# Kernel tuning notes

Hardware: AMD Instinct MI355X
Metric: run time of the kernel (lower is better)

The kernel has to match this reference:

```python
import jax, jax.numpy as jnp
import numpy as np

TEMPERATURE = 0.5

def setup_inputs() -> dict:
    key = jax.random.key(0)
    ks = jax.random.split(key, 8)
    B, D, H, T, C = 4096, 1024, 4096, 8, 1000
    return {
        "x": jax.random.normal(ks[0], (B, D), jnp.float32),
        "signatures": jax.random.normal(ks[1], (T, D), jnp.float32) * 0.1,
        "W_up": jax.random.normal(ks[2], (T, H, D), jnp.float32) * (1.0 / np.sqrt(D)),
        "b_up": jax.random.normal(ks[3], (T, H), jnp.float32) * 0.01,
        "W_down": jax.random.normal(ks[4], (T, D, H), jnp.float32) * (1.0 / np.sqrt(H)),
        "b_down": jax.random.normal(ks[5], (T, D), jnp.float32) * 0.01,
        "W_cls": jax.random.normal(ks[6], (C, D), jnp.float32) * (1.0 / np.sqrt(D)),
        "b_cls": jax.random.normal(ks[7], (C,), jnp.float32) * 0.01,
    }

def reference(x, signatures, W_up, b_up, W_down, b_down, W_cls, b_cls):
    # Soft routing: scores (B, T), softmax weights at temperature 0.5
    scores = x @ signatures.T
    indices = jnp.argmax(scores, axis=-1)
    weights = jax.nn.softmax(scores / TEMPERATURE, axis=-1)
    # Batched per-tile FFN: Linear -> GELU(exact) -> Linear, all tiles at once
    h = jax.nn.gelu(jnp.einsum('bd,thd->bth', x, W_up) + b_up[None], approximate=False)  # (B,T,H)
    tile_out = jnp.einsum('bth,tdh->btd', h, W_down) + b_down[None]                      # (B,T,D)
    # Weighted combine + residual
    outputs = jnp.einsum('bt,btd->bd', weights, tile_out) + x
    logits = outputs @ W_cls.T + b_cls
    return logits, indices, weights
```

## Files before the change

### kernel.cpp

```cpp
#include <hip/hip_runtime.h>
#include <stdint.h>


typedef __attribute__((ext_vector_type(8))) __bf16 bf16x8;
typedef __attribute__((ext_vector_type(4))) float f32x4;

__device__ __forceinline__ unsigned short f2bf(float f) {
  union { float f; unsigned int u; } c; c.f = f;
  unsigned int u = c.u;
  u += 0x7FFFu + ((u >> 16) & 1u);
  return (unsigned short)(u >> 16);
}

__device__ __forceinline__ float gelu_fast(float x) {
  float x2 = x * x;
  float p = __builtin_fmaf(0.044715f * x2, x, x);
  float e = __expf(-1.5957691216057308f * p);
  return x / (1.0f + e);
}

__device__ __forceinline__ void gload16(const void* g, void* l) {
  __builtin_amdgcn_global_load_lds((const __attribute__((address_space(1))) void*)g,
                                   (__attribute__((address_space(3))) void*)l,
                                   16, 0, 0);
}

__global__ void conv_bf16(const float* __restrict__ in, unsigned short* __restrict__ out, int n4) {
  int i = blockIdx.x * blockDim.x + threadIdx.x;
  if (i >= n4) return;
  float4 v = reinterpret_cast<const float4*>(in)[i];
  ushort4 o;
  o.x = f2bf(v.x); o.y = f2bf(v.y); o.z = f2bf(v.z); o.w = f2bf(v.w);
  reinterpret_cast<ushort4*>(out)[i] = o;
}

__global__ void conv_wdn(const float* __restrict__ in, unsigned short* __restrict__ out) {
  int i = blockIdx.x * blockDim.x + threadIdx.x;
  int idx = i * 4;
  int h = idx & 4095;
  int d = (idx >> 12) & 1023;
  int t = idx >> 22;
  float4 v = *reinterpret_cast<const float4*>(in + (size_t)(t * 1024 + d) * 4096 + h);
  ushort4 o;
  o.x = f2bf(v.x); o.y = f2bf(v.y); o.z = f2bf(v.z); o.w = f2bf(v.w);
  *reinterpret_cast<ushort4*>(out + (size_t)d * 32768 + t * 4096 + h) = o;
}

__global__ void conv_wcls(const float* __restrict__ in, unsigned short* __restrict__ out) {
  int i = blockIdx.x * blockDim.x + threadIdx.x;
  int idx = i * 4;
  int row = idx >> 10;
  float4 v = make_float4(0.f, 0.f, 0.f, 0.f);
  if (row < 1000) v = *reinterpret_cast<const float4*>(in + row * 1024 + (idx & 1023));
  ushort4 o;
  o.x = f2bf(v.x); o.y = f2bf(v.y); o.z = f2bf(v.z); o.w = f2bf(v.w);
  reinterpret_cast<ushort4*>(out)[i] = o;
}

__global__ void score_init(const float* __restrict__ x, const float* __restrict__ sig,
                           const float* __restrict__ b_down,
                           float* __restrict__ w_ws, float* __restrict__ out_init,
                           float* __restrict__ w_out, float* __restrict__ idx_out) {
  const int b = blockIdx.x;
  const int tid = threadIdx.x;
  const int lane = tid & 63;
  const int wave = tid >> 6;
  const float* xr = x + (size_t)b * 1024;

  float p[8];
  #pragma unroll
  for (int t = 0; t < 8; ++t) p[t] = 0.f;
  for (int k = tid; k < 1024; k += 256) {
    float xv = xr[k];
    #pragma unroll
    for (int t = 0; t < 8; ++t) p[t] += xv * sig[t * 1024 + k];
  }
  #pragma unroll
  for (int t = 0; t < 8; ++t) {
    #pragma unroll
    for (int off = 32; off > 0; off >>= 1) p[t] += __shfl_down(p[t], off);
  }
  __shared__ float red[4][8];
  __shared__ float wsh[8];
  if (lane == 0) {
    #pragma unroll
    for (int t = 0; t < 8; ++t) red[wave][t] = p[t];
  }
  __syncthreads();
  if (tid == 0) {
    float s[8];
    #pragma unroll
    for (int t = 0; t < 8; ++t) s[t] = red[0][t] + red[1][t] + red[2][t] + red[3][t];
    int amax = 0; float mx = s[0];
    #pragma unroll
    for (int t = 1; t < 8; ++t) { if (s[t] > mx) { mx = s[t]; amax = t; } }
    float e[8], sum = 0.f;
    #pragma unroll
    for (int t = 0; t < 8; ++t) { e[t] = expf((s[t] - mx) * 2.0f); sum += e[t]; }
    float inv = 1.0f / sum;
    #pragma unroll
    for (int t = 0; t < 8; ++t) {
      float wv = e[t] * inv;
      wsh[t] = wv;
      w_out[(size_t)b * 8 + t] = wv;
      w_ws[(size_t)b * 8 + t] = wv;
    }
    idx_out[b] = (float)amax;
  }
  __syncthreads();
  for (int d = tid; d < 1024; d += 256) {
    float acc = xr[d];
    #pragma unroll
    for (int t = 0; t < 8; ++t) acc += wsh[t] * b_down[t * 1024 + d];
    out_init[(size_t)b * 1024 + d] = acc;
  }
}

template <int MODE>
__global__ __launch_bounds__(512, 2) void gemm8(
    const unsigned short* __restrict__ A, int lda,
    const unsigned short* __restrict__ Bm, int ldb,
    float* __restrict__ Cf,
    unsigned short* __restrict__ Ch,
    const float* __restrict__ bias,
    const float* __restrict__ wcol) {
  constexpr int NU = (MODE == 0) ? 32 : 256;
  __shared__ char lds[131072];

  const int tid = threadIdx.x;
  const int f = blockIdx.x;
  int m0, n0;
  size_t koff = 0;
  if (MODE == 0) {
    int sf = (f & 7) * 256 + (f >> 3);
    n0 = (sf >> 4) * 256;
    m0 = (sf & 15) * 256;
  } else {
    int sf = (f & 7) * 32 + (f >> 3);
    int z = sf >> 6, rem = sf & 63;
    m0 = (rem >> 2) * 256;
    n0 = (rem & 3) * 256;
    koff = (size_t)z * 8192;
    Cf += (size_t)z * 4194304;
  }

  const int srow = tid >> 2;
  const int selB = ((tid & 3) << 4) ^ (((tid >> 3) & 3) << 4);
  const unsigned short* Ag = A + (size_t)(m0 + srow) * lda + koff + (selB >> 1);
  const unsigned short* Bg = Bm + (size_t)(n0 + srow) * ldb + koff + (selB >> 1);
  const size_t ldaH = (size_t)128 * lda, ldbH = (size_t)128 * ldb;
  char* const ldsA = lds + tid * 16;
  char* const ldsB = lds + 65536 + tid * 16;

  const int lane = tid & 63;
  const int wave = tid >> 6;
  const int lr = lane & 15, lg = lane >> 4;
  const int wm = (wave >> 2) * 128;
  const int wn = (wave & 3) * 64;

  int offA[8], offB[4];
  #pragma unroll
  for (int mi = 0; mi < 8; ++mi) {
    int r = wm + mi * 16 + lr;
    offA[mi] = r * 64 + ((lg << 4) ^ (((r >> 1) & 3) << 4));
  }
  #pragma unroll
  for (int ni = 0; ni < 4; ++ni) {
    int r = wn + ni * 16 + lr;
    offB[ni] = r * 64 + ((lg << 4) ^ (((r >> 1) & 3) << 4));
  }
  const char* const ldsRA = lds;
  const char* const ldsRB = lds + 65536;

  f32x4 acc[8][4];
  #pragma unroll
  for (int i = 0; i < 8; ++i)
    #pragma unroll
    for (int j = 0; j < 4; ++j)
      #pragma unroll
      for (int q = 0; q < 4; ++q) acc[i][j][q] = 0.f;

#define STAGE(u_)                                                        \
  {                                                                      \
    const int s_ = ((u_) & 3) * 16384;                                   \
    const size_t kel_ = (size_t)(u_) * 32;                               \
    gload16(Ag + kel_,        ldsA + s_);                                \
    gload16(Ag + ldaH + kel_, ldsA + s_ + 8192);                         \
    gload16(Bg + kel_,        ldsB + s_);                                \
    gload16(Bg + ldbH + kel_, ldsB + s_ + 8192);                         \
  }

#define PHASES(u_, doStage)                                              \
  {                                                                      \
    const int s_ = ((u_) & 3) * 16384;                                   \
    bf16x8 av[4], bv[4];                                                 \
    _Pragma("unroll")                                                    \
    for (int ni = 0; ni < 4; ++ni)                                       \
      bv[ni] = *(const bf16x8*)(ldsRB + s_ + offB[ni]);                  \
    _Pragma("unroll")                                                    \
    for (int j = 0; j < 4; ++j)                                          \
      av[j] = *(const bf16x8*)(ldsRA + s_ + offA[j]);                    \
    if (doStage) STAGE((u_) + 3)                                         \
    asm volatile("s_waitcnt lgkmcnt(0)" ::: "memory");                   \
    __builtin_amdgcn_sched_barrier(0);                                   \
    __builtin_amdgcn_s_setprio(1);                                       \
    _Pragma("unroll")                                                    \
    for (int j = 0; j < 4; ++j)                                          \
      _Pragma("unroll")                                                  \
      for (int ni = 0; ni < 4; ++ni)                                     \
        acc[j][ni] = __builtin_amdgcn_mfma_f32_16x16x32_bf16(            \
            av[j], bv[ni], acc[j][ni], 0, 0, 0);                         \
    __builtin_amdgcn_s_setprio(0);                                       \
    __builtin_amdgcn_s_barrier();                                        \
    _Pragma("unroll")                                                    \
    for (int j = 0; j < 4; ++j)                                          \
      av[j] = *(const bf16x8*)(ldsRA + s_ + offA[4 + j]);                \
    asm volatile("s_waitcnt lgkmcnt(0)" ::: "memory");                   \
    __builtin_amdgcn_sched_barrier(0);                                   \
    __builtin_amdgcn_s_setprio(1);                                       \
    _Pragma("unroll")                                                    \
    for (int j = 0; j < 4; ++j)                                          \
      _Pragma("unroll")                                                  \
      for (int ni = 0; ni < 4; ++ni)                                     \
        acc[4 + j][ni] = __builtin_amdgcn_mfma_f32_16x16x32_bf16(        \
            av[j], bv[ni], acc[4 + j][ni], 0, 0, 0);                     \
    __builtin_amdgcn_s_setprio(0);                                       \
  }

  STAGE(0) STAGE(1) STAGE(2)

  #pragma unroll 4
  for (int u = 0; u < NU - 2; ++u) {
    asm volatile("s_waitcnt vmcnt(8)" ::: "memory");
    __builtin_amdgcn_s_barrier();
    PHASES(u, (u < NU - 3))
  }
  asm volatile("s_waitcnt vmcnt(4)" ::: "memory");
  __builtin_amdgcn_s_barrier();
  PHASES(NU - 2, false)
  asm volatile("s_waitcnt vmcnt(0)" ::: "memory");
  __builtin_amdgcn_s_barrier();
  PHASES(NU - 1, false)

#undef STAGE
#undef PHASES

  #pragma unroll
  for (int mi = 0; mi < 8; ++mi) {
    float wr[4];
    if (MODE == 0) {
      #pragma unroll
      for (int r = 0; r < 4; ++r)
        wr[r] = wcol[(size_t)(m0 + wm + mi * 16 + lg * 4 + r) * 8 + (n0 >> 12)];
    }
    #pragma unroll
    for (int ni = 0; ni < 4; ++ni) {
      int gn = n0 + wn + ni * 16 + lr;
      #pragma unroll
      for (int r = 0; r < 4; ++r) {
        int gm = m0 + wm + mi * 16 + lg * 4 + r;
        float v = acc[mi][ni][r];
        if (MODE == 0) {
          v += bias[gn];
          v = gelu_fast(v) * wr[r];
          Ch[(size_t)gm * 32768 + gn] = f2bf(v);
        } else {
          Cf[(size_t)gm * 1024 + gn] = v;
        }
      }
    }
  }
}

template <int BN>
__global__ __launch_bounds__(256, 2) void gemm_cls(
    const unsigned short* __restrict__ A, int lda,
    const unsigned short* __restrict__ Bm, int ldb,
    int K, float* __restrict__ Cf, int ldc, int nvalid,
    const float* __restrict__ bias) {
  constexpr int FN = BN / 32;
  __shared__ unsigned short As[128 * 64];
  __shared__ unsigned short Bs[BN * 64];

  const int tid = threadIdx.x;
  const int lane = tid & 63;
  const int wave = tid >> 6;
  const int m0 = blockIdx.y * 128;
  const int n0 = blockIdx.x * BN;
  const int lr = lane & 15;
  const int lg = lane >> 4;
  const int wm = (wave >> 1) * 64;
  const int wn = (wave & 1) * (BN / 2);
  const int sw = (lr & 7) << 4;

  f32x4 acc[4][FN];
  #pragma unroll
  for (int i = 0; i < 4; ++i)
    #pragma unroll
    for (int j = 0; j < FN; ++j)
      #pragma unroll
      for (int q = 0; q < 4; ++q) acc[i][j][q] = 0.f;

  const char* Ab = (const char*)As;
  const char* Bb = (const char*)Bs;
  const int Lw = wave * 1024 + lane * 16;

  for (int k0 = 0; k0 < K; k0 += 64) {
    #pragma unroll
    for (int it = 0; it < 4; ++it) {
      int L = it * 4096 + Lw;
      int row = L >> 7;
      int cb = (L & 127) ^ ((row & 7) << 4);
      gload16(A + (size_t)(m0 + row) * lda + k0 + (cb >> 1),
              (void*)((char*)As + it * 4096 + wave * 1024));
    }
    #pragma unroll
    for (int it = 0; it < FN; ++it) {
      int L = it * 4096 + Lw;
      int row = L >> 7;
      int cb = (L & 127) ^ ((row & 7) << 4);
      gload16(Bm + (size_t)(n0 + row) * ldb + k0 + (cb >> 1),
              (void*)((char*)Bs + it * 4096 + wave * 1024));
    }
    asm volatile("s_waitcnt vmcnt(0)" ::: "memory");
    __syncthreads();

    #pragma unroll
    for (int kk = 0; kk < 2; ++kk) {
      bf16x8 a[4], bfr[FN];
      const int cbase = (kk << 6) + (lg << 4);
      #pragma unroll
      for (int mi = 0; mi < 4; ++mi)
        a[mi] = *(const bf16x8*)(Ab + ((wm + mi * 16 + lr) << 7) + (cbase ^ sw));
      #pragma unroll
      for (int ni = 0; ni < FN; ++ni)
        bfr[ni] = *(const bf16x8*)(Bb + ((wn + ni * 16 + lr) << 7) + (cbase ^ sw));
      #pragma unroll
      for (int mi = 0; mi < 4; ++mi)
        #pragma unroll
        for (int ni = 0; ni < FN; ++ni)
          acc[mi][ni] = __builtin_amdgcn_mfma_f32_16x16x32_bf16(a[mi], bfr[ni], acc[mi][ni], 0, 0, 0);
    }
    __syncthreads();
  }

  #pragma unroll
  for (int mi = 0; mi < 4; ++mi)
    #pragma unroll
    for (int ni = 0; ni < FN; ++ni) {
      int gn = n0 + wn + ni * 16 + lr;
      #pragma unroll
      for (int r = 0; r < 4; ++r) {
        int gm = m0 + wm + mi * 16 + lg * 4 + r;
        if (gn < nvalid) Cf[(size_t)gm * ldc + gn] = acc[mi][ni][r] + bias[gn];
      }
    }
}

__global__ void combine_k(const float* __restrict__ init, const float* __restrict__ parts,
                          unsigned short* __restrict__ out) {
  int i = blockIdx.x * blockDim.x + threadIdx.x;
  float4 s = reinterpret_cast<const float4*>(init)[i];
  #pragma unroll
  for (int z = 0; z < 4; ++z) {
    float4 p = reinterpret_cast<const float4*>(parts + (size_t)z * 4194304)[i];
    s.x += p.x; s.y += p.y; s.z += p.z; s.w += p.w;
  }
  ushort4 o;
  o.x = f2bf(s.x); o.y = f2bf(s.y); o.z = f2bf(s.z); o.w = f2bf(s.w);
  reinterpret_cast<ushort4*>(out)[i] = o;
}

extern "C" void kernel_launch(void* const* d_in, const int* in_sizes, int n_in,
                              void* d_out, int out_size, void* d_ws, size_t ws_size,
                              hipStream_t stream) {
  const float* x      = (const float*)d_in[0];
  const float* sig    = (const float*)d_in[1];
  const float* W_up   = (const float*)d_in[2];
  const float* b_up   = (const float*)d_in[3];
  const float* W_down = (const float*)d_in[4];
  const float* b_down = (const float*)d_in[5];
  const float* W_cls  = (const float*)d_in[6];
  const float* b_cls  = (const float*)d_in[7];

  float* outp    = (float*)d_out;
  float* logits  = outp;
  float* idx_out = outp + 4096000;
  float* w_out   = outp + 4096000 + 4096;

  char* ws = (char*)d_ws;
  unsigned short* xb    = (unsigned short*)ws;  ws += 8388608;
  unsigned short* hsc   = (unsigned short*)ws;  ws += 268435456;
  unsigned short* wupb  = (unsigned short*)ws;  ws += 67108864;
  unsigned short* wdnb  = (unsigned short*)ws;  ws += 67108864;
  unsigned short* wclsb = (unsigned short*)ws;  ws += 2097152;
  unsigned short* outb  = (unsigned short*)ws;  ws += 8388608;
  float* out_init       = (float*)ws;           ws += 16777216;
  float* parts          = (float*)ws;           ws += 67108864;
  float* w_ws           = (float*)ws;           ws += 131072;

  dim3 blk(256);

  conv_bf16<<<dim3(4096), blk, 0, stream>>>(x, xb, 1048576);
  score_init<<<dim3(4096), blk, 0, stream>>>(x, sig, b_down, w_ws, out_init, w_out, idx_out);
  conv_bf16<<<dim3(32768), blk, 0, stream>>>(W_up, wupb, 8388608);
  conv_wdn<<<dim3(32768), blk, 0, stream>>>(W_down, wdnb);
  conv_wcls<<<dim3(1024), blk, 0, stream>>>(W_cls, wclsb);

  gemm8<0><<<dim3(2048), dim3(512), 0, stream>>>(
      xb, 1024, wupb, 1024, (float*)nullptr, hsc, b_up, w_ws);

  gemm8<1><<<dim3(256), dim3(512), 0, stream>>>(
      hsc, 32768, wdnb, 32768, parts, (unsigned short*)nullptr,
      (const float*)nullptr, (const float*)nullptr);

  combine_k<<<dim3(4096), blk, 0, stream>>>(out_init, parts, outb);

  gemm_cls<64><<<dim3(16, 32), blk, 0, stream>>>(
      outb, 1024, wclsb, 1024, 1024, logits, 1000, 1000, b_cls);
}
```

Before: 795.1 us.

## Double-buffer LDS fragment registers to overlap reads with MFMA in GEMM loop

Restructures the GEMM main loop so LDS fragment reads for the next k-step go into a second register set while MFMAs run on the current set. This replaces the old two-phase scheme with an intra-step barrier and lgkmcnt wait. The aim is to hide LDS read latency behind matrix math and drop one barrier per step. It doubles fragment register usage (24 bf16x8 vectors), which may raise register pressure and reduce occupancy, and it assumes NU is even with NU >= 4.

```diff
diff --git a/kernel.cpp b/kernel.cpp
--- a/kernel.cpp
+++ b/kernel.cpp
@@ -167,10 +167,8 @@
   #pragma unroll
   for (int ni = 0; ni < 4; ++ni) {
     int r = wn + ni * 16 + lr;
-    offB[ni] = r * 64 + ((lg << 4) ^ (((r >> 1) & 3) << 4));
-  }
-  const char* const ldsRA = lds;
-  const char* const ldsRB = lds + 65536;
+    offB[ni] = 65536 + r * 64 + ((lg << 4) ^ (((r >> 1) & 3) << 4));
+  }
 
   f32x4 acc[8][4];
   #pragma unroll
@@ -179,6 +177,8 @@
     for (int j = 0; j < 4; ++j)
       #pragma unroll
       for (int q = 0; q < 4; ++q) acc[i][j][q] = 0.f;
+
+  bf16x8 avP[8], bvP[4], avQ[8], bvQ[4];
 
 #define STAGE(u_)                                                        \
   {                                                                      \
@@ -190,60 +190,82 @@
     gload16(Bg + ldbH + kel_, ldsB + s_ + 8192);                         \
   }
 
-#define PHASES(u_, doStage)                                              \
+#define READS(av_, bv_, u_)                                              \
   {                                                                      \
-    const int s_ = ((u_) & 3) * 16384;                                   \
-    bf16x8 av[4], bv[4];                                                 \
+    const char* b_ = lds + (((u_) & 3) * 16384);                         \
     _Pragma("unroll")                                                    \
     for (int ni = 0; ni < 4; ++ni)                                       \
-      bv[ni] = *(const bf16x8*)(ldsRB + s_ + offB[ni]);                  \
+      bv_[ni] = *(const bf16x8*)(b_ + offB[ni]);                         \
     _Pragma("unroll")                                                    \
-    for (int j = 0; j < 4; ++j)                                          \
-      av[j] = *(const bf16x8*)(ldsRA + s_ + offA[j]);                    \
-    if (doStage) STAGE((u_) + 3)                                         \
-    asm volatile("s_waitcnt lgkmcnt(0)" ::: "memory");                   \
-    __builtin_amdgcn_sched_barrier(0);                                   \
-    __builtin_amdgcn_s_setprio(1);                                       \
+    for (int mi = 0; mi < 8; ++mi)                                       \
+      av_[mi] = *(const bf16x8*)(b_ + offA[mi]);                         \
+  }
+
+#define MFMA32(av_, bv_)                                                 \
+  __builtin_amdgcn_s_setprio(1);                                         \
+  _Pragma("unroll")                                                      \
+  for (int mi = 0; mi < 8; ++mi)                                         \
     _Pragma("unroll")                                                    \
-    for (int j = 0; j < 4; ++j)                                          \
-      _Pragma("unroll")                                                  \
-      for (int ni = 0; ni < 4; ++ni)                                     \
-        acc[j][ni] = __builtin_amdgcn_mfma_f32_16x16x32_bf16(            \
-            av[j], bv[ni], acc[j][ni], 0, 0, 0);                         \
-    __builtin_amdgcn_s_setprio(0);                                       \
-    __builtin_amdgcn_s_barrier();                                        \
-    _Pragma("unroll")                                                    \
-    for (int j = 0; j < 4; ++j)                                          \
-      av[j] = *(const bf16x8*)(ldsRA + s_ + offA[4 + j]);                \
-    asm volatile("s_waitcnt lgkmcnt(0)" ::: "memory");                   \
-    __builtin_amdgcn_sched_barrier(0);                                   \
-    __builtin_amdgcn_s_setprio(1);                                       \
-    _Pragma("unroll")                                                    \
-    for (int j = 0; j < 4; ++j)                                          \
-      _Pragma("unroll")                                                  \
-      for (int ni = 0; ni < 4; ++ni)                                     \
-        acc[4 + j][ni] = __builtin_amdgcn_mfma_f32_16x16x32_bf16(        \
-            av[j], bv[ni], acc[4 + j][ni], 0, 0, 0);                     \
-    __builtin_amdgcn_s_setprio(0);                                       \
-  }
+    for (int ni = 0; ni < 4; ++ni)                                       \
+      acc[mi][ni] = __builtin_amdgcn_mfma_f32_16x16x32_bf16(             \
+          av_[mi], bv_[ni], acc[mi][ni], 0, 0, 0);                       \
+  __builtin_amdgcn_s_setprio(0);
+
+#define VM8  asm volatile("s_waitcnt vmcnt(8)" ::: "memory");
+#define VM4  asm volatile("s_waitcnt vmcnt(4)" ::: "memory");
+#define VM0  asm volatile("s_waitcnt vmcnt(0)" ::: "memory");
+#define LG0  asm volatile("s_waitcnt lgkmcnt(0)" ::: "memory");          \
+             __builtin_amdgcn_sched_barrier(0);
+#define SB   __builtin_amdgcn_sched_barrier(0);
+#define BAR  __builtin_amdgcn_s_barrier();
 
   STAGE(0) STAGE(1) STAGE(2)
-
-  #pragma unroll 4
-  for (int u = 0; u < NU - 2; ++u) {
-    asm volatile("s_waitcnt vmcnt(8)" ::: "memory");
-    __builtin_amdgcn_s_barrier();
-    PHASES(u, (u < NU - 3))
-  }
-  asm volatile("s_waitcnt vmcnt(4)" ::: "memory");
-  __builtin_amdgcn_s_barrier();
-  PHASES(NU - 2, false)
-  asm volatile("s_waitcnt vmcnt(0)" ::: "memory");
-  __builtin_amdgcn_s_barrier();
-  PHASES(NU - 1, false)
+  VM8 BAR
+  READS(avP, bvP, 0)
+  STAGE(3)
+  LG0
+
+  #pragma unroll 2
+  for (int u = 0; u < NU - 4; u += 2) {
+    VM8 BAR
+    READS(avQ, bvQ, u + 1)
+    STAGE(u + 4)
+    SB
+    MFMA32(avP, bvP)
+    LG0
+    VM8 BAR
+    READS(avP, bvP, u + 2)
+    STAGE(u + 5)
+    SB
+    MFMA32(avQ, bvQ)
+    LG0
+  }
+  VM8 BAR
+  READS(avQ, bvQ, NU - 3)
+  SB
+  MFMA32(avP, bvP)
+  LG0
+  VM4 BAR
+  READS(avP, bvP, NU - 2)
+  SB
+  MFMA32(avQ, bvQ)
+  LG0
+  VM0 BAR
+  READS(avQ, bvQ, NU - 1)
+  SB
+  MFMA32(avP, bvP)
+  LG0
+  MFMA32(avQ, bvQ)
 
 #undef STAGE
-#undef PHASES
+#undef READS
+#undef MFMA32
+#undef VM8
+#undef VM4
+#undef VM0
+#undef LG0
+#undef SB
+#undef BAR
 
   #pragma unroll
   for (int mi = 0; mi < 8; ++mi) {
```

Result: slower. 906.3 us (+14.0%).

## Replace 256x256 eight-wave GEMM with 128x128 four-wave tiled kernel

Applied to the files above, without the earlier changes.

Both FFN GEMMs switch from a 256x256-tile, 512-thread kernel with split MFMA phases, priority hints and XCD-aware block swizzling to a 128x128-tile, 256-thread kernel. The new kernel has a plain 4-stage LDS ring and a direct 2D/3D grid. Smaller tiles cut LDS and registers per block and give more blocks for scheduling. In exchange each block reuses data less, so global and LDS traffic per FLOP rises, and L2 locality from the swizzle is lost.

```diff
diff --git a/kernel.cpp b/kernel.cpp
--- a/kernel.cpp
+++ b/kernel.cpp
@@ -116,139 +116,119 @@
   }
 }
 
-template <int MODE>
-__global__ __launch_bounds__(512, 2) void gemm8(
+template <int EPI>
+__global__ __launch_bounds__(256, 2) void gemm_r4(
     const unsigned short* __restrict__ A, int lda,
     const unsigned short* __restrict__ Bm, int ldb,
     float* __restrict__ Cf,
     unsigned short* __restrict__ Ch,
     const float* __restrict__ bias,
     const float* __restrict__ wcol) {
-  constexpr int NU = (MODE == 0) ? 32 : 256;
-  __shared__ char lds[131072];
+  constexpr int NU = (EPI == 0) ? 32 : 256;
+  __shared__ char lds[65536];
 
   const int tid = threadIdx.x;
-  const int f = blockIdx.x;
   int m0, n0;
   size_t koff = 0;
-  if (MODE == 0) {
-    int sf = (f & 7) * 256 + (f >> 3);
-    n0 = (sf >> 4) * 256;
-    m0 = (sf & 15) * 256;
+  if (EPI == 0) {
+    n0 = blockIdx.x * 128;
+    m0 = blockIdx.y * 128;
   } else {
-    int sf = (f & 7) * 32 + (f >> 3);
-    int z = sf >> 6, rem = sf & 63;
-    m0 = (rem >> 2) * 256;
-    n0 = (rem & 3) * 256;
-    koff = (size_t)z * 8192;
-    Cf += (size_t)z * 4194304;
+    m0 = blockIdx.x * 128;
+    n0 = blockIdx.y * 128;
+    koff = (size_t)blockIdx.z * 8192;
+    Cf += (size_t)blockIdx.z * 4194304;
   }
 
   const int srow = tid >> 2;
-  const int selB = ((tid & 3) << 4) ^ (((tid >> 3) & 3) << 4);
-  const unsigned short* Ag = A + (size_t)(m0 + srow) * lda + koff + (selB >> 1);
-  const unsigned short* Bg = Bm + (size_t)(n0 + srow) * ldb + koff + (selB >> 1);
-  const size_t ldaH = (size_t)128 * lda, ldbH = (size_t)128 * ldb;
+  const int scb = ((tid & 3) << 4) ^ ((srow & 3) << 4);
+  const unsigned short* Ag = A + (size_t)(m0 + srow) * lda + koff + (scb >> 1);
+  const unsigned short* Bg = Bm + (size_t)(n0 + srow) * ldb + koff + (scb >> 1);
+  const size_t ldaH = (size_t)64 * lda, ldbH = (size_t)64 * ldb;
   char* const ldsA = lds + tid * 16;
-  char* const ldsB = lds + 65536 + tid * 16;
+  char* const ldsB = lds + 32768 + tid * 16;
 
   const int lane = tid & 63;
   const int wave = tid >> 6;
   const int lr = lane & 15, lg = lane >> 4;
-  const int wm = (wave >> 2) * 128;
-  const int wn = (wave & 3) * 64;
-
-  int offA[8], offB[4];
-  #pragma unroll
-  for (int mi = 0; mi < 8; ++mi) {
+  const int wm = (wave >> 1) * 64;
+  const int wn = (wave & 1) * 64;
+
+  int offA[4], offB[4];
+  #pragma unroll
+  for (int mi = 0; mi < 4; ++mi) {
     int r = wm + mi * 16 + lr;
-    offA[mi] = r * 64 + ((lg << 4) ^ (((r >> 1) & 3) << 4));
+    offA[mi] = r * 64 + ((lg << 4) ^ ((r & 3) << 4));
   }
   #pragma unroll
   for (int ni = 0; ni < 4; ++ni) {
     int r = wn + ni * 16 + lr;
-    offB[ni] = r * 64 + ((lg << 4) ^ (((r >> 1) & 3) << 4));
-  }
-  const char* const ldsRA = lds;
-  const char* const ldsRB = lds + 65536;
-
-  f32x4 acc[8][4];
-  #pragma unroll
-  for (int i = 0; i < 8; ++i)
+    offB[ni] = 32768 + r * 64 + ((lg << 4) ^ ((r & 3) << 4));
+  }
+
+  f32x4 acc[4][4];
+  #pragma unroll
+  for (int i = 0; i < 4; ++i)
     #pragma unroll
     for (int j = 0; j < 4; ++j)
       #pragma unroll
       for (int q = 0; q < 4; ++q) acc[i][j][q] = 0.f;
 
-#define STAGE(u_)                                                        \
+#define STAGE(u_, s_)                                                    \
   {                                                                      \
-    const int s_ = ((u_) & 3) * 16384;                                   \
     const size_t kel_ = (size_t)(u_) * 32;                               \
-    gload16(Ag + kel_,        ldsA + s_);                                \
-    gload16(Ag + ldaH + kel_, ldsA + s_ + 8192);                         \
-    gload16(Bg + kel_,        ldsB + s_);                                \
-    gload16(Bg + ldbH + kel_, ldsB + s_ + 8192);                         \
-  }
-
-#define PHASES(u_, doStage)                                              \
+    gload16(Ag + kel_,        ldsA + (s_) * 8192);                       \
+    gload16(Ag + ldaH + kel_, ldsA + (s_) * 8192 + 4096);                \
+    gload16(Bg + kel_,        ldsB + (s_) * 8192);                       \
+    gload16(Bg + ldbH + kel_, ldsB + (s_) * 8192 + 4096);                \
+  }
+
+#define COMP(s_)                                                         \
   {                                                                      \
-    const int s_ = ((u_) & 3) * 16384;                                   \
-    bf16x8 av[4], bv[4];                                                 \
+    bf16x8 a[4], b[4];                                                   \
+    _Pragma("unroll")                                                    \
+    for (int mi = 0; mi < 4; ++mi)                                       \
+      a[mi] = *(const bf16x8*)(lds + (s_) * 8192 + offA[mi]);            \
     _Pragma("unroll")                                                    \
     for (int ni = 0; ni < 4; ++ni)                                       \
-      bv[ni] = *(const bf16x8*)(ldsRB + s_ + offB[ni]);                  \
+      b[ni] = *(const bf16x8*)(lds + (s_) * 8192 + offB[ni]);            \
     _Pragma("unroll")                                                    \
-    for (int j = 0; j < 4; ++j)                                          \
-      av[j] = *(const bf16x8*)(ldsRA + s_ + offA[j]);                    \
-    if (doStage) STAGE((u_) + 3)                                         \
-    asm volatile("s_waitcnt lgkmcnt(0)" ::: "memory");                   \
-    __builtin_amdgcn_sched_barrier(0);                                   \
-    __builtin_amdgcn_s_setprio(1);                                       \
-    _Pragma("unroll")                                                    \
-    for (int j = 0; j < 4; ++j)                                          \
+    for (int mi = 0; mi < 4; ++mi)                                       \
       _Pragma("unroll")                                                  \
       for (int ni = 0; ni < 4; ++ni)                                     \
-        acc[j][ni] = __builtin_amdgcn_mfma_f32_16x16x32_bf16(            \
-            av[j], bv[ni], acc[j][ni], 0, 0, 0);                         \
-    __builtin_amdgcn_s_setprio(0);                                       \
-    __builtin_amdgcn_s_barrier();                                        \
-    _Pragma("unroll")                                                    \
-    for (int j = 0; j < 4; ++j)                                          \
-      av[j] = *(const bf16x8*)(ldsRA + s_ + offA[4 + j]);                \
-    asm volatile("s_waitcnt lgkmcnt(0)" ::: "memory");                   \
-    __builtin_amdgcn_sched_barrier(0);                                   \
-    __builtin_amdgcn_s_setprio(1);                                       \
-    _Pragma("unroll")                                                    \
-    for (int j = 0; j < 4; ++j)                                          \
-      _Pragma("unroll")                                                  \
-      for (int ni = 0; ni < 4; ++ni)                                     \
-        acc[4 + j][ni] = __builtin_amdgcn_mfma_f32_16x16x32_bf16(        \
-            av[j], bv[ni], acc[4 + j][ni], 0, 0, 0);                     \
-    __builtin_amdgcn_s_setprio(0);                                       \
-  }
-
-  STAGE(0) STAGE(1) STAGE(2)
-
-  #pragma unroll 4
-  for (int u = 0; u < NU - 2; ++u) {
-    asm volatile("s_waitcnt vmcnt(8)" ::: "memory");
-    __builtin_amdgcn_s_barrier();
-    PHASES(u, (u < NU - 3))
-  }
-  asm volatile("s_waitcnt vmcnt(4)" ::: "memory");
-  __builtin_amdgcn_s_barrier();
-  PHASES(NU - 2, false)
-  asm volatile("s_waitcnt vmcnt(0)" ::: "memory");
-  __builtin_amdgcn_s_barrier();
-  PHASES(NU - 1, false)
+        acc[mi][ni] = __builtin_amdgcn_mfma_f32_16x16x32_bf16(           \
+            a[mi], b[ni], acc[mi][ni], 0, 0, 0);                         \
+  }
+
+#define VM8  asm volatile("s_waitcnt vmcnt(8)" ::: "memory");
+#define VM4  asm volatile("s_waitcnt vmcnt(4)" ::: "memory");
+#define VM0  asm volatile("s_waitcnt vmcnt(0)" ::: "memory");
+#define BARR asm volatile("s_barrier" ::: "memory");
+
+  STAGE(0, 0) STAGE(1, 1) STAGE(2, 2)
+
+  for (int u = 0; u < NU - 4; u += 4) {
+    VM8 BARR STAGE(u + 3, 3) COMP(0)
+    VM8 BARR STAGE(u + 4, 0) COMP(1)
+    VM8 BARR STAGE(u + 5, 1) COMP(2)
+    VM8 BARR STAGE(u + 6, 2) COMP(3)
+  }
+  VM8 BARR STAGE(NU - 1, 3) COMP(0)
+  VM8 BARR COMP(1)
+  VM4 BARR COMP(2)
+  VM0 BARR COMP(3)
 
 #undef STAGE
-#undef PHASES
-
-  #pragma unroll
-  for (int mi = 0; mi < 8; ++mi) {
+#undef COMP
+#undef VM8
+#undef VM4
+#undef VM0
+#undef BARR
+
+  #pragma unroll
+  for (int mi = 0; mi < 4; ++mi) {
     float wr[4];
-    if (MODE == 0) {
+    if (EPI == 0) {
       #pragma unroll
       for (int r = 0; r < 4; ++r)
         wr[r] = wcol[(size_t)(m0 + wm + mi * 16 + lg * 4 + r) * 8 + (n0 >> 12)];
@@ -260,7 +240,7 @@
       for (int r = 0; r < 4; ++r) {
         int gm = m0 + wm + mi * 16 + lg * 4 + r;
         float v = acc[mi][ni][r];
-        if (MODE == 0) {
+        if (EPI == 0) {
           v += bias[gn];
           v = gelu_fast(v) * wr[r];
           Ch[(size_t)gm * 32768 + gn] = f2bf(v);
@@ -407,10 +387,10 @@
   conv_wdn<<<dim3(32768), blk, 0, stream>>>(W_down, wdnb);
   conv_wcls<<<dim3(1024), blk, 0, stream>>>(W_cls, wclsb);
 
-  gemm8<0><<<dim3(2048), dim3(512), 0, stream>>>(
+  gemm_r4<0><<<dim3(256, 32), blk, 0, stream>>>(
       xb, 1024, wupb, 1024, (float*)nullptr, hsc, b_up, w_ws);
 
-  gemm8<1><<<dim3(256), dim3(512), 0, stream>>>(
+  gemm_r4<3><<<dim3(32, 8, 4), blk, 0, stream>>>(
       hsc, 32768, wdnb, 32768, parts, (unsigned short*)nullptr,
       (const float*)nullptr, (const float*)nullptr);
 
```

Measured after the change: 913.4 us. 1.15x slower.
